# Kernel optimization log

Hardware: AMD Instinct MI355X
Metric: run time of the kernel (lower is better)

## Reference

```python
import jax, jax.numpy as jnp
import numpy as np

NUM_TAGS = 9
INNER_DIM = 64
HIDDEN = 768
MASK_VAL = 1e12


def setup_inputs() -> dict:
    key = jax.random.key(0)
    k1, k2, k3, k4 = jax.random.split(key, 4)
    B, S = 16, 512
    encoder_output = jax.random.normal(k1, (B, S, HIDDEN), dtype=jnp.float32)
    token_ids = jax.random.randint(k2, (B, S), 0, 30000, dtype=jnp.int64)
    attention_mask = jnp.ones((B, S), dtype=jnp.int32)
    W = jax.random.normal(k3, (HIDDEN, NUM_TAGS * INNER_DIM * 2), dtype=jnp.float32) * 0.02
    b = jax.random.normal(k4, (NUM_TAGS * INNER_DIM * 2,), dtype=jnp.float32) * 0.02
    return {"encoder_output": encoder_output, "token_ids": token_ids,
            "attention_mask": attention_mask, "W": W, "b": b}


def _rope_sin_cos(seq_len, dim, dtype):
    # sinusoidal position embedding, interleaved then repeat_interleave(2)
    pos = jnp.arange(seq_len, dtype=dtype)[:, None]              # [S,1]
    inv = jnp.power(10000.0, -2.0 * jnp.arange(dim // 2, dtype=dtype) / dim)
    ang = pos * inv                                              # [S,d/2]
    sin = jnp.repeat(jnp.sin(ang), 2, axis=-1)                   # [S,d]
    cos = jnp.repeat(jnp.cos(ang), 2, axis=-1)                   # [S,d]
    return sin, cos


def _rotate_half(x):
    # stack([-x[...,1::2], x[...,::2]], -1).reshape(x.shape)
    x2 = jnp.stack([-x[..., 1::2], x[..., ::2]], axis=-1)
    return x2.reshape(x.shape)


def reference(encoder_output, token_ids, attention_mask, W, b):
    B, S, _ = encoder_output.shape
    d = INNER_DIM
    out = encoder_output @ W + b                                 # [B,S,T*2d]
    out = out.reshape(B, S, NUM_TAGS, 2 * d)
    qw, kw = out[..., :d], out[..., d:]                          # [B,S,T,d]

    sin, cos = _rope_sin_cos(S, d, encoder_output.dtype)
    sin = sin[None, :, None, :]                                  # [1,S,1,d]
    cos = cos[None, :, None, :]
    qw = qw * cos + _rotate_half(qw) * sin
    kw = kw * cos + _rotate_half(kw) * sin

    logits = jnp.einsum('bshd,bthd->bhst', qw, kw)               # [B,T,S,S]

    pad = attention_mask.astype(logits.dtype)[:, None, None, :]  # key-side mask
    logits = logits * pad - (1.0 - pad) * MASK_VAL
    tril = jnp.tril(jnp.ones((S, S), dtype=logits.dtype), -1)
    logits = logits - tril * MASK_VAL
    return logits / jnp.sqrt(jnp.asarray(d, logits.dtype))
```

## Files before the change

### kernel.cpp

```cpp
#include <hip/hip_runtime.h>

#define MASK_VALF 1000000000000.0f

typedef __attribute__((ext_vector_type(8))) short s16x8;
typedef __attribute__((ext_vector_type(4))) float f32x4;
typedef __attribute__((ext_vector_type(16))) float f32x16;

__device__ __forceinline__ unsigned f2bf_u(float f) {
    union { float f; unsigned u; } v; v.f = f;
    return (v.u + 0x7FFFu + ((v.u >> 16) & 1u)) >> 16;
}
__device__ __forceinline__ short f2bf(float f) { return (short)(f2bf_u(f) & 0xFFFFu); }

#define GLOAD16(gp, lp) __builtin_amdgcn_global_load_lds( \
    (const __attribute__((address_space(1))) void*)(gp),  \
    (__attribute__((address_space(3))) void*)(lp), 16, 0, 0)

__global__ __launch_bounds__(256) void prep_all(
    const float* __restrict__ enc, short* __restrict__ encb,
    const float* __restrict__ W, short* __restrict__ wtb,
    float* __restrict__ scf)
{
    const int blk = blockIdx.x;
    const int t = threadIdx.x;
    if (blk < 6144) {
        int i = blk * 256 + t;
        float4 v = ((const float4*)enc)[i];
        short4 o;
        o.x = f2bf(v.x); o.y = f2bf(v.y); o.z = f2bf(v.z); o.w = f2bf(v.w);
        ((short4*)encb)[i] = o;
    } else if (blk < 7008) {
        __shared__ float tile[32][33];
        int tb = blk - 6144;
        int tbx = tb % 36;
        int tby = tb / 36;
        int tx = t & 31, ty = t >> 5;
#pragma unroll
        for (int r = 0; r < 4; ++r) {
            int row = ty + r * 8;
            tile[row][tx] = W[(tby * 32 + row) * 1152 + tbx * 32 + tx];
        }
        __syncthreads();
#pragma unroll
        for (int r = 0; r < 4; ++r) {
            int row = ty + r * 8;
            wtb[(size_t)(tbx * 32 + row) * 768 + tby * 32 + tx] = f2bf(tile[tx][row]);
        }
    } else {
        int id = (blk - 7008) * 256 + t;
        int pos = id >> 5, j = id & 31;
        float inv = powf(10000.0f, -2.0f * (float)j / 64.0f);
        float ang = (float)pos * inv;
        float s, c;
        sincosf(ang, &s, &c);
        scf[id * 2]     = c;
        scf[id * 2 + 1] = s;
    }
}

__global__ __launch_bounds__(256) void gemm1_rope(
    const short* __restrict__ A,
    const short* __restrict__ Bt,
    const float* __restrict__ bias,
    const float* __restrict__ scf,
    short* __restrict__ qk)
{
    __shared__ __align__(16) short As[2][128 * 32];
    __shared__ __align__(16) short Bs[2][128 * 32];
    const int t = threadIdx.x;
    const int w = t >> 6, lane = t & 63;
    const int l31 = lane & 31, lh = lane >> 5;
    const int wn2 = w & 1, wm2 = w >> 1;
    const int m0 = blockIdx.y * 128;
    const int n0 = blockIdx.x * 128;

    f32x16 acc[2][2] = {};

    const short* gA = A  + (size_t)(m0 + (t >> 2)) * 768 + (t & 3) * 8;
    const short* gB = Bt + (size_t)(n0 + (t >> 2)) * 768 + (t & 3) * 8;

    GLOAD16(gA,            &As[0][w * 512]);
    GLOAD16(gA + 64 * 768, &As[0][2048 + w * 512]);
    GLOAD16(gB,            &Bs[0][w * 512]);
    GLOAD16(gB + 64 * 768, &Bs[0][2048 + w * 512]);
    gA += 32; gB += 32;

    auto compute = [&](const short* as, const short* bs) {
        s16x8 af[2][2], bf[2][2];
#pragma unroll
        for (int fi = 0; fi < 2; ++fi)
#pragma unroll
            for (int kk = 0; kk < 2; ++kk) {
                af[fi][kk] = *(const s16x8*)&bs[(wn2 * 64 + fi * 32 + l31) * 32 + kk * 16 + lh * 8];
                bf[fi][kk] = *(const s16x8*)&as[(wm2 * 64 + fi * 32 + l31) * 32 + kk * 16 + lh * 8];
            }
#pragma unroll
        for (int kk = 0; kk < 2; ++kk)
#pragma unroll
            for (int fi = 0; fi < 2; ++fi)
#pragma unroll
                for (int fj = 0; fj < 2; ++fj)
                    acc[fi][fj] = __builtin_amdgcn_mfma_f32_32x32x16_bf16(
                        af[fi][kk], bf[fj][kk], acc[fi][fj], 0, 0, 0);
    };

    for (int kt = 0; kt < 23; ++kt) {
        __syncthreads();
        const int cur = kt & 1, nxt = cur ^ 1;
        GLOAD16(gA,            &As[nxt][w * 512]);
        GLOAD16(gA + 64 * 768, &As[nxt][2048 + w * 512]);
        GLOAD16(gB,            &Bs[nxt][w * 512]);
        GLOAD16(gB + 64 * 768, &Bs[nxt][2048 + w * 512]);
        gA += 32; gB += 32;
        compute(As[cur], Bs[cur]);
    }
    __syncthreads();
    compute(As[1], Bs[1]);

#pragma unroll
    for (int fi = 0; fi < 2; ++fi) {
        const int n_base = n0 + wn2 * 64 + fi * 32;
#pragma unroll
        for (int fj = 0; fj < 2; ++fj) {
            const int rowg = m0 + wm2 * 64 + fj * 32 + l31;
            const int bidx = rowg >> 9;
            const int pos  = rowg & 511;
#pragma unroll
            for (int g = 0; g < 4; ++g) {
                const int colg0 = n_base + g * 8 + lh * 4;
                const float4 bv = *(const float4*)&bias[colg0];
                const int tag = colg0 >> 7;
                const int qkf = (colg0 >> 6) & 1;
                const int dd0 = colg0 & 63;
                const float4 cs = *(const float4*)&scf[pos * 64 + dd0];
                float x0 = acc[fi][fj][g * 4 + 0] + bv.x;
                float x1 = acc[fi][fj][g * 4 + 1] + bv.y;
                float x2 = acc[fi][fj][g * 4 + 2] + bv.z;
                float x3 = acc[fi][fj][g * 4 + 3] + bv.w;
                float o0 = x0 * cs.x - x1 * cs.y;
                float o1 = x1 * cs.x + x0 * cs.y;
                float o2 = x2 * cs.z - x3 * cs.w;
                float o3 = x3 * cs.z + x2 * cs.w;
                int2 st;
                st.x = (int)(f2bf_u(o0) & 0xFFFFu) | (int)(f2bf_u(o1) << 16);
                st.y = (int)(f2bf_u(o2) & 0xFFFFu) | (int)(f2bf_u(o3) << 16);
                *(int2*)&qk[((((size_t)bidx * 9 + tag) * 2 + qkf) * 512 + pos) * 64 + dd0] = st;
            }
        }
    }
}

__global__ __launch_bounds__(256) void gemm2_mask(
    const short* __restrict__ qk,
    const int* __restrict__ amask,
    float* __restrict__ out)
{
    __shared__ __align__(16) short Qs[128 * 64];
    __shared__ __align__(16) short Ks[128 * 64];
    const int t = threadIdx.x;
    const int w = t >> 6, lane = t & 63;
    const int lr = lane & 15, quad = lane >> 4;
    const int wm = w >> 1, wn = w & 1;
    const int bh = blockIdx.z;
    const int bidx = bh / 9;
    const int s0 = blockIdx.y * 128;
    const int t0 = blockIdx.x * 128;

    const short* qbase = qk + (size_t)bh * 2 * 512 * 64;
    const short* kbase = qbase + 512 * 64;

    const int row = t >> 3, col8 = (t & 7) * 8;
#pragma unroll
    for (int p = 0; p < 4; ++p) {
        GLOAD16(qbase + (size_t)(s0 + p * 32 + row) * 64 + col8, &Qs[p * 2048 + w * 512]);
        GLOAD16(kbase + (size_t)(t0 + p * 32 + row) * 64 + col8, &Ks[p * 2048 + w * 512]);
    }
    __syncthreads();

    f32x4 acc[4][4] = {};
#pragma unroll
    for (int kk = 0; kk < 64; kk += 32) {
        s16x8 af[4], bw[4];
#pragma unroll
        for (int i = 0; i < 4; ++i)
            af[i] = *(const s16x8*)&Ks[(wm * 64 + i * 16 + lr) * 64 + kk + quad * 8];
#pragma unroll
        for (int j = 0; j < 4; ++j)
            bw[j] = *(const s16x8*)&Qs[(wn * 64 + j * 16 + lr) * 64 + kk + quad * 8];
#pragma unroll
        for (int i = 0; i < 4; ++i)
#pragma unroll
            for (int j = 0; j < 4; ++j)
                acc[i][j] = __builtin_amdgcn_mfma_f32_16x16x32_bf16(af[i], bw[j], acc[i][j], 0, 0, 0);
    }

#pragma unroll
    for (int i = 0; i < 4; ++i) {
        const int tg0 = t0 + wm * 64 + i * 16 + quad * 4;
        const int4 am = *(const int4*)&amask[bidx * 512 + tg0];
        const float4 pad = make_float4((float)am.x, (float)am.y, (float)am.z, (float)am.w);
        const float4 mk = make_float4((1.0f - pad.x) * MASK_VALF, (1.0f - pad.y) * MASK_VALF,
                                      (1.0f - pad.z) * MASK_VALF, (1.0f - pad.w) * MASK_VALF);
#pragma unroll
        for (int j = 0; j < 4; ++j) {
            const int sg = s0 + wn * 64 + j * 16 + lr;
            float4 v;
            v.x = (acc[i][j][0] * pad.x - mk.x - (sg > tg0     ? MASK_VALF : 0.0f)) * 0.125f;
            v.y = (acc[i][j][1] * pad.y - mk.y - (sg > tg0 + 1 ? MASK_VALF : 0.0f)) * 0.125f;
            v.z = (acc[i][j][2] * pad.z - mk.z - (sg > tg0 + 2 ? MASK_VALF : 0.0f)) * 0.125f;
            v.w = (acc[i][j][3] * pad.w - mk.w - (sg > tg0 + 3 ? MASK_VALF : 0.0f)) * 0.125f;
            *(float4*)&out[((size_t)bh * 512 + sg) * 512 + tg0] = v;
        }
    }
}

extern "C" void kernel_launch(void* const* d_in, const int* in_sizes, int n_in,
                              void* d_out, int out_size, void* d_ws, size_t ws_size,
                              hipStream_t stream) {
    const float* enc   = (const float*)d_in[0];
    const int*   amask = (const int*)d_in[2];
    const float* W     = (const float*)d_in[3];
    const float* bias  = (const float*)d_in[4];
    float* out = (float*)d_out;

    char* ws = (char*)d_ws;
    short* encb = (short*)(ws);
    short* wtb  = (short*)(ws + 12582912);
    float* scf  = (float*)(ws + 14352384);
    short* qk   = (short*)(ws + 14483456);

    prep_all  <<<7072, 256, 0, stream>>>(enc, encb, W, wtb, scf);
    gemm1_rope<<<dim3(9, 64), 256, 0, stream>>>(encb, wtb, bias, scf, qk);
    gemm2_mask<<<dim3(4, 4, 144), 256, 0, stream>>>(qk, amask, out);
}
```

Baseline: 229.1 us.

## Fuse prep, GEMM1 and GEMM2 into one persistent kernel with grid barriers

Merges the three kernel launches into one persistent kernel of 576 blocks. Blocks loop over the conversion jobs, meet at a software grid barrier, run the projection GEMM with RoPE (one tile per block), meet again, then loop over the QK^T masked-output tiles. The aim is to remove launch gaps and tail effects between kernels. In exchange it adds atomic-barrier spin costs and a memset launch, and it relies on all 576 blocks being co-resident, which is needed to avoid deadlock.

```diff
diff --git a/kernel.cpp b/kernel.cpp
--- a/kernel.cpp
+++ b/kernel.cpp
@@ -1,6 +1,7 @@
 #include <hip/hip_runtime.h>
 
 #define MASK_VALF 1000000000000.0f
+#define NBLK 576
 
 typedef __attribute__((ext_vector_type(8))) short s16x8;
 typedef __attribute__((ext_vector_type(4))) float f32x4;
@@ -16,200 +17,225 @@
     (const __attribute__((address_space(1))) void*)(gp),  \
     (__attribute__((address_space(3))) void*)(lp), 16, 0, 0)
 
-__global__ __launch_bounds__(256) void prep_all(
-    const float* __restrict__ enc, short* __restrict__ encb,
-    const float* __restrict__ W, short* __restrict__ wtb,
-    float* __restrict__ scf)
-{
-    const int blk = blockIdx.x;
-    const int t = threadIdx.x;
-    if (blk < 6144) {
-        int i = blk * 256 + t;
-        float4 v = ((const float4*)enc)[i];
-        short4 o;
-        o.x = f2bf(v.x); o.y = f2bf(v.y); o.z = f2bf(v.z); o.w = f2bf(v.w);
-        ((short4*)encb)[i] = o;
-    } else if (blk < 7008) {
-        __shared__ float tile[32][33];
-        int tb = blk - 6144;
-        int tbx = tb % 36;
-        int tby = tb / 36;
-        int tx = t & 31, ty = t >> 5;
-#pragma unroll
-        for (int r = 0; r < 4; ++r) {
-            int row = ty + r * 8;
-            tile[row][tx] = W[(tby * 32 + row) * 1152 + tbx * 32 + tx];
-        }
-        __syncthreads();
-#pragma unroll
-        for (int r = 0; r < 4; ++r) {
-            int row = ty + r * 8;
-            wtb[(size_t)(tbx * 32 + row) * 768 + tby * 32 + tx] = f2bf(tile[tx][row]);
-        }
-    } else {
-        int id = (blk - 7008) * 256 + t;
-        int pos = id >> 5, j = id & 31;
-        float inv = powf(10000.0f, -2.0f * (float)j / 64.0f);
-        float ang = (float)pos * inv;
-        float s, c;
-        sincosf(ang, &s, &c);
-        scf[id * 2]     = c;
-        scf[id * 2 + 1] = s;
-    }
-}
-
-__global__ __launch_bounds__(256) void gemm1_rope(
-    const short* __restrict__ A,
-    const short* __restrict__ Bt,
+__device__ __forceinline__ void grid_sync(unsigned* bar) {
+    __syncthreads();
+    if (threadIdx.x == 0) {
+        __threadfence();
+        unsigned gen = __hip_atomic_load(&bar[1], __ATOMIC_RELAXED, __HIP_MEMORY_SCOPE_AGENT);
+        unsigned arrived = __hip_atomic_fetch_add(&bar[0], 1u, __ATOMIC_ACQ_REL, __HIP_MEMORY_SCOPE_AGENT);
+        if (arrived == gridDim.x - 1) {
+            __hip_atomic_store(&bar[0], 0u, __ATOMIC_RELAXED, __HIP_MEMORY_SCOPE_AGENT);
+            __hip_atomic_fetch_add(&bar[1], 1u, __ATOMIC_RELEASE, __HIP_MEMORY_SCOPE_AGENT);
+        } else {
+            while (__hip_atomic_load(&bar[1], __ATOMIC_RELAXED, __HIP_MEMORY_SCOPE_AGENT) == gen)
+                __builtin_amdgcn_s_sleep(8);
+        }
+        __threadfence();
+    }
+    __syncthreads();
+}
+
+__global__ __launch_bounds__(256, 3) void fused_all(
+    const float* __restrict__ enc,
+    const float* __restrict__ W,
     const float* __restrict__ bias,
-    const float* __restrict__ scf,
-    short* __restrict__ qk)
-{
-    __shared__ __align__(16) short As[2][128 * 32];
-    __shared__ __align__(16) short Bs[2][128 * 32];
-    const int t = threadIdx.x;
-    const int w = t >> 6, lane = t & 63;
-    const int l31 = lane & 31, lh = lane >> 5;
-    const int wn2 = w & 1, wm2 = w >> 1;
-    const int m0 = blockIdx.y * 128;
-    const int n0 = blockIdx.x * 128;
-
-    f32x16 acc[2][2] = {};
-
-    const short* gA = A  + (size_t)(m0 + (t >> 2)) * 768 + (t & 3) * 8;
-    const short* gB = Bt + (size_t)(n0 + (t >> 2)) * 768 + (t & 3) * 8;
-
-    GLOAD16(gA,            &As[0][w * 512]);
-    GLOAD16(gA + 64 * 768, &As[0][2048 + w * 512]);
-    GLOAD16(gB,            &Bs[0][w * 512]);
-    GLOAD16(gB + 64 * 768, &Bs[0][2048 + w * 512]);
-    gA += 32; gB += 32;
-
-    auto compute = [&](const short* as, const short* bs) {
-        s16x8 af[2][2], bf[2][2];
-#pragma unroll
-        for (int fi = 0; fi < 2; ++fi)
-#pragma unroll
-            for (int kk = 0; kk < 2; ++kk) {
-                af[fi][kk] = *(const s16x8*)&bs[(wn2 * 64 + fi * 32 + l31) * 32 + kk * 16 + lh * 8];
-                bf[fi][kk] = *(const s16x8*)&as[(wm2 * 64 + fi * 32 + l31) * 32 + kk * 16 + lh * 8];
-            }
-#pragma unroll
-        for (int kk = 0; kk < 2; ++kk)
-#pragma unroll
-            for (int fi = 0; fi < 2; ++fi)
-#pragma unroll
-                for (int fj = 0; fj < 2; ++fj)
-                    acc[fi][fj] = __builtin_amdgcn_mfma_f32_32x32x16_bf16(
-                        af[fi][kk], bf[fj][kk], acc[fi][fj], 0, 0, 0);
-    };
-
-    for (int kt = 0; kt < 23; ++kt) {
-        __syncthreads();
-        const int cur = kt & 1, nxt = cur ^ 1;
-        GLOAD16(gA,            &As[nxt][w * 512]);
-        GLOAD16(gA + 64 * 768, &As[nxt][2048 + w * 512]);
-        GLOAD16(gB,            &Bs[nxt][w * 512]);
-        GLOAD16(gB + 64 * 768, &Bs[nxt][2048 + w * 512]);
-        gA += 32; gB += 32;
-        compute(As[cur], Bs[cur]);
-    }
-    __syncthreads();
-    compute(As[1], Bs[1]);
-
-#pragma unroll
-    for (int fi = 0; fi < 2; ++fi) {
-        const int n_base = n0 + wn2 * 64 + fi * 32;
-#pragma unroll
-        for (int fj = 0; fj < 2; ++fj) {
-            const int rowg = m0 + wm2 * 64 + fj * 32 + l31;
-            const int bidx = rowg >> 9;
-            const int pos  = rowg & 511;
-#pragma unroll
-            for (int g = 0; g < 4; ++g) {
-                const int colg0 = n_base + g * 8 + lh * 4;
-                const float4 bv = *(const float4*)&bias[colg0];
-                const int tag = colg0 >> 7;
-                const int qkf = (colg0 >> 6) & 1;
-                const int dd0 = colg0 & 63;
-                const float4 cs = *(const float4*)&scf[pos * 64 + dd0];
-                float x0 = acc[fi][fj][g * 4 + 0] + bv.x;
-                float x1 = acc[fi][fj][g * 4 + 1] + bv.y;
-                float x2 = acc[fi][fj][g * 4 + 2] + bv.z;
-                float x3 = acc[fi][fj][g * 4 + 3] + bv.w;
-                float o0 = x0 * cs.x - x1 * cs.y;
-                float o1 = x1 * cs.x + x0 * cs.y;
-                float o2 = x2 * cs.z - x3 * cs.w;
-                float o3 = x3 * cs.z + x2 * cs.w;
-                int2 st;
-                st.x = (int)(f2bf_u(o0) & 0xFFFFu) | (int)(f2bf_u(o1) << 16);
-                st.y = (int)(f2bf_u(o2) & 0xFFFFu) | (int)(f2bf_u(o3) << 16);
-                *(int2*)&qk[((((size_t)bidx * 9 + tag) * 2 + qkf) * 512 + pos) * 64 + dd0] = st;
-            }
-        }
-    }
-}
-
-__global__ __launch_bounds__(256) void gemm2_mask(
-    const short* __restrict__ qk,
-    const int* __restrict__ amask,
+    const int*   __restrict__ amask,
+    short* __restrict__ encb,
+    short* __restrict__ wtb,
+    float* __restrict__ scf,
+    short* __restrict__ qk,
+    unsigned* __restrict__ bar,
     float* __restrict__ out)
 {
-    __shared__ __align__(16) short Qs[128 * 64];
-    __shared__ __align__(16) short Ks[128 * 64];
+    __shared__ __align__(16) char smem[32768];
     const int t = threadIdx.x;
-    const int w = t >> 6, lane = t & 63;
-    const int lr = lane & 15, quad = lane >> 4;
-    const int wm = w >> 1, wn = w & 1;
-    const int bh = blockIdx.z;
-    const int bidx = bh / 9;
-    const int s0 = blockIdx.y * 128;
-    const int t0 = blockIdx.x * 128;
-
-    const short* qbase = qk + (size_t)bh * 2 * 512 * 64;
-    const short* kbase = qbase + 512 * 64;
-
-    const int row = t >> 3, col8 = (t & 7) * 8;
-#pragma unroll
-    for (int p = 0; p < 4; ++p) {
-        GLOAD16(qbase + (size_t)(s0 + p * 32 + row) * 64 + col8, &Qs[p * 2048 + w * 512]);
-        GLOAD16(kbase + (size_t)(t0 + p * 32 + row) * 64 + col8, &Ks[p * 2048 + w * 512]);
-    }
-    __syncthreads();
-
-    f32x4 acc[4][4] = {};
-#pragma unroll
-    for (int kk = 0; kk < 64; kk += 32) {
-        s16x8 af[4], bw[4];
-#pragma unroll
-        for (int i = 0; i < 4; ++i)
-            af[i] = *(const s16x8*)&Ks[(wm * 64 + i * 16 + lr) * 64 + kk + quad * 8];
-#pragma unroll
-        for (int j = 0; j < 4; ++j)
-            bw[j] = *(const s16x8*)&Qs[(wn * 64 + j * 16 + lr) * 64 + kk + quad * 8];
-#pragma unroll
-        for (int i = 0; i < 4; ++i)
-#pragma unroll
-            for (int j = 0; j < 4; ++j)
-                acc[i][j] = __builtin_amdgcn_mfma_f32_16x16x32_bf16(af[i], bw[j], acc[i][j], 0, 0, 0);
-    }
-
-#pragma unroll
-    for (int i = 0; i < 4; ++i) {
-        const int tg0 = t0 + wm * 64 + i * 16 + quad * 4;
-        const int4 am = *(const int4*)&amask[bidx * 512 + tg0];
-        const float4 pad = make_float4((float)am.x, (float)am.y, (float)am.z, (float)am.w);
-        const float4 mk = make_float4((1.0f - pad.x) * MASK_VALF, (1.0f - pad.y) * MASK_VALF,
-                                      (1.0f - pad.z) * MASK_VALF, (1.0f - pad.w) * MASK_VALF);
-#pragma unroll
-        for (int j = 0; j < 4; ++j) {
-            const int sg = s0 + wn * 64 + j * 16 + lr;
-            float4 v;
-            v.x = (acc[i][j][0] * pad.x - mk.x - (sg > tg0     ? MASK_VALF : 0.0f)) * 0.125f;
-            v.y = (acc[i][j][1] * pad.y - mk.y - (sg > tg0 + 1 ? MASK_VALF : 0.0f)) * 0.125f;
-            v.z = (acc[i][j][2] * pad.z - mk.z - (sg > tg0 + 2 ? MASK_VALF : 0.0f)) * 0.125f;
-            v.w = (acc[i][j][3] * pad.w - mk.w - (sg > tg0 + 3 ? MASK_VALF : 0.0f)) * 0.125f;
-            *(float4*)&out[((size_t)bh * 512 + sg) * 512 + tg0] = v;
+
+    for (int job = blockIdx.x; job < 7072; job += NBLK) {
+        if (job < 6144) {
+            int i = job * 256 + t;
+            float4 v = ((const float4*)enc)[i];
+            short4 o;
+            o.x = f2bf(v.x); o.y = f2bf(v.y); o.z = f2bf(v.z); o.w = f2bf(v.w);
+            ((short4*)encb)[i] = o;
+        } else if (job < 7008) {
+            float (*tile)[33] = (float(*)[33])smem;
+            int tb = job - 6144;
+            int tbx = tb % 36;
+            int tby = tb / 36;
+            int tx = t & 31, ty = t >> 5;
+            __syncthreads();
+#pragma unroll
+            for (int r = 0; r < 4; ++r) {
+                int row = ty + r * 8;
+                tile[row][tx] = W[(tby * 32 + row) * 1152 + tbx * 32 + tx];
+            }
+            __syncthreads();
+#pragma unroll
+            for (int r = 0; r < 4; ++r) {
+                int row = ty + r * 8;
+                wtb[(size_t)(tbx * 32 + row) * 768 + tby * 32 + tx] = f2bf(tile[tx][row]);
+            }
+        } else {
+            int id = (job - 7008) * 256 + t;
+            int pos = id >> 5, j = id & 31;
+            float inv = powf(10000.0f, -2.0f * (float)j / 64.0f);
+            float ang = (float)pos * inv;
+            float s, c;
+            sincosf(ang, &s, &c);
+            scf[id * 2]     = c;
+            scf[id * 2 + 1] = s;
+        }
+    }
+
+    grid_sync(bar);
+
+    {
+        short* As = (short*)smem;
+        short* Bs = (short*)(smem + 16384);
+        const int w = t >> 6, lane = t & 63;
+        const int l31 = lane & 31, lh = lane >> 5;
+        const int wn2 = w & 1, wm2 = w >> 1;
+        const int m0 = (blockIdx.x / 9) * 128;
+        const int n0 = (blockIdx.x % 9) * 128;
+
+        f32x16 acc[2][2] = {};
+
+        const short* gA = encb + (size_t)(m0 + (t >> 2)) * 768 + (t & 3) * 8;
+        const short* gB = wtb  + (size_t)(n0 + (t >> 2)) * 768 + (t & 3) * 8;
+
+        GLOAD16(gA,            As + w * 512);
+        GLOAD16(gA + 64 * 768, As + 2048 + w * 512);
+        GLOAD16(gB,            Bs + w * 512);
+        GLOAD16(gB + 64 * 768, Bs + 2048 + w * 512);
+        gA += 32; gB += 32;
+
+        auto compute = [&](const short* as, const short* bs) {
+            s16x8 af[2][2], bf[2][2];
+#pragma unroll
+            for (int fi = 0; fi < 2; ++fi)
+#pragma unroll
+                for (int kk = 0; kk < 2; ++kk) {
+                    af[fi][kk] = *(const s16x8*)&bs[(wn2 * 64 + fi * 32 + l31) * 32 + kk * 16 + lh * 8];
+                    bf[fi][kk] = *(const s16x8*)&as[(wm2 * 64 + fi * 32 + l31) * 32 + kk * 16 + lh * 8];
+                }
+#pragma unroll
+            for (int kk = 0; kk < 2; ++kk)
+#pragma unroll
+                for (int fi = 0; fi < 2; ++fi)
+#pragma unroll
+                    for (int fj = 0; fj < 2; ++fj)
+                        acc[fi][fj] = __builtin_amdgcn_mfma_f32_32x32x16_bf16(
+                            af[fi][kk], bf[fj][kk], acc[fi][fj], 0, 0, 0);
+        };
+
+        for (int kt = 0; kt < 23; ++kt) {
+            __syncthreads();
+            const int cur = kt & 1, nxt = cur ^ 1;
+            GLOAD16(gA,            As + nxt * 4096 + w * 512);
+            GLOAD16(gA + 64 * 768, As + nxt * 4096 + 2048 + w * 512);
+            GLOAD16(gB,            Bs + nxt * 4096 + w * 512);
+            GLOAD16(gB + 64 * 768, Bs + nxt * 4096 + 2048 + w * 512);
+            gA += 32; gB += 32;
+            compute(As + cur * 4096, Bs + cur * 4096);
+        }
+        __syncthreads();
+        compute(As + 4096, Bs + 4096);
+
+#pragma unroll
+        for (int fi = 0; fi < 2; ++fi) {
+            const int n_base = n0 + wn2 * 64 + fi * 32;
+#pragma unroll
+            for (int fj = 0; fj < 2; ++fj) {
+                const int rowg = m0 + wm2 * 64 + fj * 32 + l31;
+                const int bidx = rowg >> 9;
+                const int pos  = rowg & 511;
+#pragma unroll
+                for (int g = 0; g < 4; ++g) {
+                    const int colg0 = n_base + g * 8 + lh * 4;
+                    const float4 bv = *(const float4*)&bias[colg0];
+                    const int tag = colg0 >> 7;
+                    const int qkf = (colg0 >> 6) & 1;
+                    const int dd0 = colg0 & 63;
+                    const float4 cs = *(const float4*)&scf[pos * 64 + dd0];
+                    float x0 = acc[fi][fj][g * 4 + 0] + bv.x;
+                    float x1 = acc[fi][fj][g * 4 + 1] + bv.y;
+                    float x2 = acc[fi][fj][g * 4 + 2] + bv.z;
+                    float x3 = acc[fi][fj][g * 4 + 3] + bv.w;
+                    float o0 = x0 * cs.x - x1 * cs.y;
+                    float o1 = x1 * cs.x + x0 * cs.y;
+                    float o2 = x2 * cs.z - x3 * cs.w;
+                    float o3 = x3 * cs.z + x2 * cs.w;
+                    int2 st;
+                    st.x = (int)(f2bf_u(o0) & 0xFFFFu) | (int)(f2bf_u(o1) << 16);
+                    st.y = (int)(f2bf_u(o2) & 0xFFFFu) | (int)(f2bf_u(o3) << 16);
+                    *(int2*)&qk[((((size_t)bidx * 9 + tag) * 2 + qkf) * 512 + pos) * 64 + dd0] = st;
+                }
+            }
+        }
+    }
+
+    grid_sync(bar);
+
+    {
+        short* Qs = (short*)smem;
+        short* Ks = (short*)(smem + 16384);
+        const int w = t >> 6, lane = t & 63;
+        const int lr = lane & 15, quad = lane >> 4;
+        const int wm = w >> 1, wn = w & 1;
+        const int row = t >> 3, col8 = (t & 7) * 8;
+
+        for (int job = blockIdx.x; job < 2304; job += NBLK) {
+            const int t0 = (job & 3) * 128;
+            const int s0 = ((job >> 2) & 3) * 128;
+            const int bh = job >> 4;
+            const int bidx = bh / 9;
+
+            const short* qbase = qk + (size_t)bh * 2 * 512 * 64;
+            const short* kbase = qbase + 512 * 64;
+
+            __syncthreads();
+#pragma unroll
+            for (int p = 0; p < 4; ++p) {
+                GLOAD16(qbase + (size_t)(s0 + p * 32 + row) * 64 + col8, Qs + p * 2048 + w * 512);
+                GLOAD16(kbase + (size_t)(t0 + p * 32 + row) * 64 + col8, Ks + p * 2048 + w * 512);
+            }
+            __syncthreads();
+
+            f32x4 acc[4][4] = {};
+#pragma unroll
+            for (int kk = 0; kk < 64; kk += 32) {
+                s16x8 af[4], bw[4];
+#pragma unroll
+                for (int i = 0; i < 4; ++i)
+                    af[i] = *(const s16x8*)&Ks[(wm * 64 + i * 16 + lr) * 64 + kk + quad * 8];
+#pragma unroll
+                for (int j = 0; j < 4; ++j)
+                    bw[j] = *(const s16x8*)&Qs[(wn * 64 + j * 16 + lr) * 64 + kk + quad * 8];
+#pragma unroll
+                for (int i = 0; i < 4; ++i)
+#pragma unroll
+                    for (int j = 0; j < 4; ++j)
+                        acc[i][j] = __builtin_amdgcn_mfma_f32_16x16x32_bf16(af[i], bw[j], acc[i][j], 0, 0, 0);
+            }
+
+#pragma unroll
+            for (int i = 0; i < 4; ++i) {
+                const int tg0 = t0 + wm * 64 + i * 16 + quad * 4;
+                const int4 am = *(const int4*)&amask[bidx * 512 + tg0];
+                const float4 pad = make_float4((float)am.x, (float)am.y, (float)am.z, (float)am.w);
+                const float4 mk = make_float4((1.0f - pad.x) * MASK_VALF, (1.0f - pad.y) * MASK_VALF,
+                                              (1.0f - pad.z) * MASK_VALF, (1.0f - pad.w) * MASK_VALF);
+#pragma unroll
+                for (int j = 0; j < 4; ++j) {
+                    const int sg = s0 + wn * 64 + j * 16 + lr;
+                    float4 v;
+                    v.x = (acc[i][j][0] * pad.x - mk.x - (sg > tg0     ? MASK_VALF : 0.0f)) * 0.125f;
+                    v.y = (acc[i][j][1] * pad.y - mk.y - (sg > tg0 + 1 ? MASK_VALF : 0.0f)) * 0.125f;
+                    v.z = (acc[i][j][2] * pad.z - mk.z - (sg > tg0 + 2 ? MASK_VALF : 0.0f)) * 0.125f;
+                    v.w = (acc[i][j][3] * pad.w - mk.w - (sg > tg0 + 3 ? MASK_VALF : 0.0f)) * 0.125f;
+                    *(float4*)&out[((size_t)bh * 512 + sg) * 512 + tg0] = v;
+                }
+            }
         }
     }
 }
@@ -224,12 +250,12 @@
     float* out = (float*)d_out;
 
     char* ws = (char*)d_ws;
-    short* encb = (short*)(ws);
-    short* wtb  = (short*)(ws + 12582912);
-    float* scf  = (float*)(ws + 14352384);
-    short* qk   = (short*)(ws + 14483456);
-
-    prep_all  <<<7072, 256, 0, stream>>>(enc, encb, W, wtb, scf);
-    gemm1_rope<<<dim3(9, 64), 256, 0, stream>>>(encb, wtb, bias, scf, qk);
-    gemm2_mask<<<dim3(4, 4, 144), 256, 0, stream>>>(qk, amask, out);
-}
+    short*    encb = (short*)(ws);
+    short*    wtb  = (short*)(ws + 12582912);
+    float*    scf  = (float*)(ws + 14352384);
+    short*    qk   = (short*)(ws + 14483456);
+    unsigned* bar  = (unsigned*)(ws + 33357824);
+
+    hipMemsetAsync(bar, 0, 2 * sizeof(unsigned), stream);
+    fused_all<<<NBLK, 256, 0, stream>>>(enc, W, bias, amask, encb, wtb, scf, qk, bar, out);
+}
```

Result: slower. 406.1 us (+77.3%).
